# Optimization experiments

Measured on AMD Instinct MI355X. Metric: run time of the kernel, lower is better.

The kernel has to match this reference:

```python
import jax, jax.numpy as jnp
import numpy as np

THRESHOLD = 0.5
EPS = 1e-6


def setup_inputs() -> dict:
    key = jax.random.key(0)
    k1, k2 = jax.random.split(key)
    points = jax.random.normal(k1, (16, 10, 30, 2), dtype=jnp.float32)
    polys = jax.random.normal(k2, (16, 16, 200, 2), dtype=jnp.float32)
    return {"points": points, "drivable_multipolygon": polys}


def reference(points, drivable_multipolygon):
    # points: (B, C, T, 2); drivable_multipolygon: (B, K, N, 2)
    # Broadcast layout: (B, K, C, T, N-1, ...)
    ps = drivable_multipolygon[:, :, None, None, :-1, :]   # edge starts (B,K,1,1,N-1,2)
    pe = drivable_multipolygon[:, :, None, None, 1:, :]    # edge ends   (B,K,1,1,N-1,2)
    pts = points[:, None, :, :, None, :]                   # (B,1,C,T,1,2)

    # --- point-to-segment distance ---
    v1 = pts - ps
    ev = pe - ps
    dot = jnp.sum(v1 * ev, axis=-1)
    esq = jnp.sum(ev * ev, axis=-1)
    proj = jnp.clip(dot / (esq + EPS), 0.0, 1.0)
    closest = ev * proj[..., None] + ps
    dist_sq = jnp.maximum(jnp.sum((pts - closest) ** 2, axis=-1), EPS)
    min_dist = jnp.min(jnp.sqrt(dist_sq), axis=-1)         # min over edges N-1 -> (B,K,C,T)
    min_dist = jnp.min(min_dist, axis=1)                   # min over polygons K -> (B,C,T)

    # --- ray-casting inside test (parity of crossings) ---
    py = pts[..., 1]
    px = pts[..., 0]
    sy, sx = ps[..., 1], ps[..., 0]
    ey, ex = pe[..., 1], pe[..., 0]
    cond_y = ((sy <= py) & (py < ey)) | ((ey <= py) & (py < sy))
    slope = (ey - sy) / (ex - sx + EPS)
    intersect_x = sx + (py - sy) / (slope + EPS)
    is_left = intersect_x > px
    intersection = cond_y & is_left                        # (B,K,C,T,N-1)
    crossings = jnp.sum(jnp.sum(intersection.astype(jnp.int32), axis=-1), axis=1)  # (B,C,T)
    inside = (crossings % 2) == 1

    min_dist = jnp.where(inside, -min_dist, min_dist)
    min_dist = jax.nn.relu(min_dist + THRESHOLD)
    return jnp.sum(min_dist, axis=-1)                      # (B, C)
```

## Files before the change

### kernel.cpp

```cpp
#include <hip/hip_runtime.h>
#include <math.h>
#include <float.h>

#define EPS 1e-6f
#define THRESHOLD 0.5f

#define NB 16
#define NPOLY 16
#define NVERT 200
#define NSEG_PER_POLY 199
#define NSEG (NPOLY * NSEG_PER_POLY)
#define NPTB 300
#define NPOINTS 4800
#define NSLICE 64
#define SEG_PER_SLICE 50

__global__ __launch_bounds__(320) void seg_kernel(
    const float* __restrict__ points,
    const float* __restrict__ polys,
    float* __restrict__ part_dsq,
    int* __restrict__ part_cross,
    float* __restrict__ out)
{
    __shared__ float4 lds[SEG_PER_SLICE * 2];

    const int slice = blockIdx.x;
    const int b     = blockIdx.y;
    const int lp    = threadIdx.x;
    const bool active = lp < NPTB;

    const int s0 = slice * SEG_PER_SLICE;
    const int s1 = (s0 + SEG_PER_SLICE < NSEG) ? s0 + SEG_PER_SLICE : NSEG;
    const int nseg = s1 - s0;

    if (lp < nseg) {
        const int s = s0 + lp;
        const int m = s / NSEG_PER_POLY;
        const int v = s % NSEG_PER_POLY;
        const float2* poly = (const float2*)polys + ((size_t)(b * NPOLY + m) * NVERT);
        const float2 S = poly[v];
        const float2 E = poly[v + 1];
        const float evx = E.x - S.x;
        const float evy = E.y - S.y;
        const float esq = evx * evx + evy * evy;
        const float inv_esq = 1.0f / (esq + EPS);
        const float slope_eps = evy / (evx + EPS) + EPS;
        const float inv_slope = __builtin_amdgcn_rcpf(slope_eps);
        lds[lp * 2]     = make_float4(S.x, S.y, evx, evy);
        lds[lp * 2 + 1] = make_float4(inv_esq, slope_eps, inv_slope, E.y);
    }
    __syncthreads();

    const int pidx = b * NPTB + (active ? lp : 0);
    const float2 pt = *(const float2*)(points + (size_t)pidx * 2);
    const float px = pt.x, py = pt.y;

    float min_dsq = FLT_MAX;
    int crossings = 0;

    #pragma unroll 2
    for (int j = 0; j < nseg; ++j) {
        const float4 p0 = lds[j * 2];
        const float4 p1 = lds[j * 2 + 1];
        const float sx = p0.x, sy = p0.y, evx = p0.z, evy = p0.w;
        const float inv_esq = p1.x, slope_eps = p1.y, inv_slope = p1.z, ey = p1.w;

        const float v1x = px - sx;
        const float v1y = py - sy;
        const float dot = v1x * evx + v1y * evy;
        float t = dot * inv_esq;
        t = fminf(fmaxf(t, 0.0f), 1.0f);
        const float dx = px - (evx * t + sx);
        const float dy = py - (evy * t + sy);
        const float dsq = dx * dx + dy * dy;
        min_dsq = fminf(min_dsq, dsq);

        const bool cond_y = (sy <= py) != (ey <= py);
        const float q    = v1y * inv_slope;
        const float ixa  = sx + q;
        const float diff = ixa - px;
        const float err  = fmaf(fabsf(q) + fabsf(ixa), 1e-6f, 1e-30f);
        bool left = diff > 0.0f;
        if (cond_y && !(fabsf(diff) > err)) {
            left = (sx + v1y / slope_eps) > px;
        }
        crossings += (cond_y && left) ? 1 : 0;
    }

    if (active) {
        const int o = slice * NPOINTS + pidx;
        part_dsq[o]   = min_dsq;
        part_cross[o] = crossings;
    } else if (slice == 0 && lp >= NPTB && lp < NPTB + 10) {
        out[b * 10 + (lp - NPTB)] = 0.0f;
    }
}

__global__ __launch_bounds__(256) void final_kernel(
    const float* __restrict__ part_dsq,
    const int* __restrict__ part_cross,
    float* __restrict__ out)
{
    const int p = blockIdx.x * 256 + threadIdx.x;
    if (p >= NPOINTS) return;

    float md = FLT_MAX;
    int c = 0;
    #pragma unroll 8
    for (int k = 0; k < NSLICE; ++k) {
        md = fminf(md, part_dsq[k * NPOINTS + p]);
        c += part_cross[k * NPOINTS + p];
    }

    float d = sqrtf(fmaxf(md, EPS));
    if (c & 1) d = -d;
    const float val = fmaxf(d + THRESHOLD, 0.0f);

    const int b = p / NPTB;
    const int a = (p % NPTB) / 30;
    atomicAdd(out + b * 10 + a, val);
}

extern "C" void kernel_launch(void* const* d_in, const int* in_sizes, int n_in,
                              void* d_out, int out_size, void* d_ws, size_t ws_size,
                              hipStream_t stream) {
    const float* points = (const float*)d_in[0];
    const float* polys  = (const float*)d_in[1];
    float* out = (float*)d_out;

    char* ws = (char*)d_ws;
    float* part_dsq   = (float*)ws;
    int*   part_cross = (int*)(ws + (2u << 20));

    dim3 grid(NSLICE, NB);
    seg_kernel<<<grid, 320, 0, stream>>>(points, polys, part_dsq, part_cross, out);
    final_kernel<<<(NPOINTS + 255) / 256, 256, 0, stream>>>(part_dsq, part_cross, out);
}
```

Baseline: 81.56 us.

## Fuse final reduction into segment kernel via last-block atomic counter

Removes the separate final reduction kernel. Each batch row keeps an atomic counter, and the last slice block to finish reduces all 64 slices' partial results and writes the per-agent sums directly. Partial results are packed as float2 pairs, and the slow exact-division fallback is skipped at wavefront level when no lane needs it. It adds a memset launch, a serialized tail reduction done by one block per batch, and a dependency on correct memory fences.

```diff
diff --git a/kernel.cpp b/kernel.cpp
--- a/kernel.cpp
+++ b/kernel.cpp
@@ -18,11 +18,13 @@
 __global__ __launch_bounds__(320) void seg_kernel(
     const float* __restrict__ points,
     const float* __restrict__ polys,
-    float* __restrict__ part_dsq,
-    int* __restrict__ part_cross,
+    float2* __restrict__ part,
+    int* __restrict__ ctr,
     float* __restrict__ out)
 {
     __shared__ float4 lds[SEG_PER_SLICE * 2];
+    __shared__ float agent_sum[10];
+    __shared__ int is_last;
 
     const int slice = blockIdx.x;
     const int b     = blockIdx.y;
@@ -81,44 +83,49 @@
         const float diff = ixa - px;
         const float err  = fmaf(fabsf(q) + fabsf(ixa), 1e-6f, 1e-30f);
         bool left = diff > 0.0f;
-        if (cond_y && !(fabsf(diff) > err)) {
-            left = (sx + v1y / slope_eps) > px;
+        const bool uncertain = cond_y && !(fabsf(diff) > err);
+        if (__ballot(uncertain)) {
+            const float ix_exact = sx + v1y / slope_eps;
+            if (uncertain) left = ix_exact > px;
         }
         crossings += (cond_y && left) ? 1 : 0;
     }
 
     if (active) {
-        const int o = slice * NPOINTS + pidx;
-        part_dsq[o]   = min_dsq;
-        part_cross[o] = crossings;
-    } else if (slice == 0 && lp >= NPTB && lp < NPTB + 10) {
-        out[b * 10 + (lp - NPTB)] = 0.0f;
+        part[slice * NPOINTS + pidx] = make_float2(min_dsq, __int_as_float(crossings));
     }
-}
+    __syncthreads();
 
-__global__ __launch_bounds__(256) void final_kernel(
-    const float* __restrict__ part_dsq,
-    const int* __restrict__ part_cross,
-    float* __restrict__ out)
-{
-    const int p = blockIdx.x * 256 + threadIdx.x;
-    if (p >= NPOINTS) return;
+    if (threadIdx.x == 0) {
+        __threadfence();
+        const int old = __hip_atomic_fetch_add(&ctr[b], 1, __ATOMIC_ACQ_REL,
+                                               __HIP_MEMORY_SCOPE_AGENT);
+        is_last = (old == NSLICE - 1) ? 1 : 0;
+        if (is_last) __threadfence();
+    }
+    __syncthreads();
+    if (!is_last) return;
 
-    float md = FLT_MAX;
-    int c = 0;
-    #pragma unroll 8
-    for (int k = 0; k < NSLICE; ++k) {
-        md = fminf(md, part_dsq[k * NPOINTS + p]);
-        c += part_cross[k * NPOINTS + p];
+    if (lp < 10) agent_sum[lp] = 0.0f;
+    __syncthreads();
+
+    if (active) {
+        float md = FLT_MAX;
+        int c = 0;
+        #pragma unroll 8
+        for (int k = 0; k < NSLICE; ++k) {
+            const float2 pr = part[k * NPOINTS + pidx];
+            md = fminf(md, pr.x);
+            c += __float_as_int(pr.y);
+        }
+        float d = sqrtf(fmaxf(md, EPS));
+        if (c & 1) d = -d;
+        const float val = fmaxf(d + THRESHOLD, 0.0f);
+        atomicAdd(&agent_sum[lp / 30], val);
     }
+    __syncthreads();
 
-    float d = sqrtf(fmaxf(md, EPS));
-    if (c & 1) d = -d;
-    const float val = fmaxf(d + THRESHOLD, 0.0f);
-
-    const int b = p / NPTB;
-    const int a = (p % NPTB) / 30;
-    atomicAdd(out + b * 10 + a, val);
+    if (lp < 10) out[b * 10 + lp] = agent_sum[lp];
 }
 
 extern "C" void kernel_launch(void* const* d_in, const int* in_sizes, int n_in,
@@ -129,10 +136,11 @@
     float* out = (float*)d_out;
 
     char* ws = (char*)d_ws;
-    float* part_dsq   = (float*)ws;
-    int*   part_cross = (int*)(ws + (2u << 20));
+    float2* part = (float2*)ws;
+    int*    ctr  = (int*)(ws + (4u << 20));
+
+    hipMemsetAsync(ctr, 0, NB * sizeof(int), stream);
 
     dim3 grid(NSLICE, NB);
-    seg_kernel<<<grid, 320, 0, stream>>>(points, polys, part_dsq, part_cross, out);
-    final_kernel<<<(NPOINTS + 255) / 256, 256, 0, stream>>>(part_dsq, part_cross, out);
+    seg_kernel<<<grid, 320, 0, stream>>>(points, polys, part, ctr, out);
 }
```

Result: slower. 114.0 us (+39.7%).
